# Kernel tuning notes

Hardware: AMD Instinct MI355X
Metric: run time of the kernel (lower is better)

Reference implementation:

```python
import jax, jax.numpy as jnp
import numpy as np

B, T, E, H = 4, 4096, 1024, 64

def setup_inputs() -> dict:
    key = jax.random.key(0)
    k1, k2, k3, k4 = jax.random.split(key, 4)
    x = jax.random.normal(k1, (B, T, E), dtype=jnp.float32)
    # nn.Linear(E, H, bias=False): weight [H, E]; store as [E, H] for x @ W
    scale = 1.0 / np.sqrt(E)
    Wk = jax.random.normal(k2, (E, H), dtype=jnp.float32) * scale
    Wq = jax.random.normal(k3, (E, H), dtype=jnp.float32) * scale
    Wv = jax.random.normal(k4, (E, H), dtype=jnp.float32) * scale
    return {"x": x, "Wk": Wk, "Wq": Wq, "Wv": Wv}

def reference(x, Wk, Wq, Wv):
    Bc, Tc, Ec = x.shape
    k = x @ Wk            # [B, T, H]
    q = x @ Wq            # [B, T, H]
    v = x @ Wv            # [B, T, H]
    # NOTE: original scales by 1/sqrt(embedding_size), not head_size
    scores = jnp.einsum('bqh,bkh->bqk', q, k) / jnp.sqrt(jnp.float32(Ec))
    causal = jnp.tril(jnp.ones((Tc, Tc), dtype=bool))
    scores = jnp.where(causal, scores, -jnp.inf)
    weights = jax.nn.softmax(scores, axis=-1)
    return jnp.einsum('bqk,bkh->bqh', weights, v)
```

## Files before the change

kernel.cpp:

```cpp
#include <hip/hip_runtime.h>

#define B_ 4
#define T_ 4096
#define E_ 1024
#define H_ 64

typedef __attribute__((ext_vector_type(8))) short short8;
typedef __attribute__((ext_vector_type(4))) float f32x4;

static __device__ __forceinline__ unsigned short f2bf(float f) {
    unsigned int u = __builtin_bit_cast(unsigned int, f);
    u += 0x7fffu + ((u >> 16) & 1u);
    return (unsigned short)(u >> 16);
}
static __device__ __forceinline__ float bf2f(unsigned short h) {
    unsigned int u = ((unsigned int)h) << 16;
    return __builtin_bit_cast(float, u);
}
#if __has_builtin(__builtin_amdgcn_exp2f)
#define EXP2(x) __builtin_amdgcn_exp2f(x)
#else
#define EXP2(x) exp2f(x)
#endif

#define GLOBAL_AS __attribute__((address_space(1)))
#define LDS_AS    __attribute__((address_space(3)))

__global__ __launch_bounds__(256) void wt_fragmajor_kernel(
    const float* __restrict__ Wq, const float* __restrict__ Wk,
    const float* __restrict__ Wv, unsigned short* __restrict__ Wtf)
{
    const int mat = blockIdx.x >> 4;
    const int kt  = blockIdx.x & 15;
    const float* W = (mat == 0) ? Wq : ((mat == 1) ? Wk : Wv);
    const int tid = threadIdx.x;
    const int col = tid & 63;
    const int kr  = tid >> 6;
    const int n   = col >> 4, c = col & 15;
    #pragma unroll
    for (int p = 0; p < 16; ++p) {
        const int k = kt * 64 + p * 4 + kr;
        const float v = W[k * 64 + col];
        const int q = k >> 5, g = (k >> 3) & 3, j = k & 7;
        Wtf[(((mat * 4 + n) * 32 + q) << 9) + (g * 16 + c) * 8 + j] = f2bf(v);
    }
}

__global__ __launch_bounds__(384, 4) void proj_kernel(
    const float* __restrict__ x, const unsigned short* __restrict__ Wtf,
    unsigned short* __restrict__ Qb, unsigned short* __restrict__ Kb,
    unsigned short* __restrict__ Vt)
{
    __shared__ float x_lds[2][2048];
    const int tid  = threadIdx.x;
    const int wid  = tid >> 6, lane = tid & 63;
    const int g    = lane >> 4, c = lane & 15;
    const int mat  = wid >> 1;
    const int rg   = wid & 1;
    const int r0   = blockIdx.x * 32;
    const float QSCALE = 0.03125f * 1.44269504088896f;

    auto stage = [&](int buf, int kk) {
        {
            int row = tid >> 4, ch = tid & 15;
            int csw = ch ^ (row & 15);
            const float* src = x + (size_t)(r0 + row) * E_ + kk + csw * 4;
            __builtin_amdgcn_global_load_lds(
                (const GLOBAL_AS unsigned int*)src,
                (LDS_AS unsigned int*)&x_lds[buf][(tid & ~63) * 4], 16, 0, 0);
        }
        if (tid < 128) {
            int idx2 = 384 + tid;
            int row2 = idx2 >> 4, ch2 = idx2 & 15;
            int csw2 = ch2 ^ (row2 & 15);
            const float* src2 = x + (size_t)(r0 + row2) * E_ + kk + csw2 * 4;
            __builtin_amdgcn_global_load_lds(
                (const GLOBAL_AS unsigned int*)src2,
                (LDS_AS unsigned int*)&x_lds[buf][(idx2 & ~63) * 4], 16, 0, 0);
        }
    };

    f32x4 acc[4];
    #pragma unroll
    for (int n = 0; n < 4; ++n) acc[n] = 0.0f;

    const int xrowbase = (rg * 16 + c) * 64;
    const unsigned short* wf = Wtf + (size_t)mat * 65536 + lane * 8;

    auto computeStep = [&](int buf, int t) {
        #pragma unroll
        for (int kc = 0; kc < 2; ++kc) {
            const int q = t * 2 + kc;
            f32x4 xa = *(const f32x4*)&x_lds[buf][xrowbase + ((8 * kc + 2 * g)     ^ c) * 4];
            f32x4 xb = *(const f32x4*)&x_lds[buf][xrowbase + ((8 * kc + 2 * g + 1) ^ c) * 4];
            short8 a;
            #pragma unroll
            for (int j = 0; j < 4; ++j) {
                a[j]     = (short)f2bf(xa[j]);
                a[j + 4] = (short)f2bf(xb[j]);
            }
            #pragma unroll
            for (int n = 0; n < 4; ++n) {
                short8 b = *(const short8*)&wf[n * 16384 + q * 512];
                acc[n] = __builtin_amdgcn_mfma_f32_16x16x32_bf16(a, b, acc[n], 0, 0, 0);
            }
        }
    };

    stage(0, 0);
    __syncthreads();
    for (int t = 0; t < 16; ++t) {
        const int buf = t & 1;
        if (t + 1 < 16) stage(buf ^ 1, (t + 1) * 64);
        computeStep(buf, t);
        __syncthreads();
    }

    const int bb = r0 >> 12;
    #pragma unroll
    for (int n = 0; n < 4; ++n)
        #pragma unroll
        for (int r = 0; r < 4; ++r) {
            int row = r0 + rg * 16 + 4 * g + r;
            int col = n * 16 + c;
            float v = acc[n][r];
            if (mat == 0)
                Qb[(size_t)row * H_ + col] = f2bf(v * QSCALE);
            else if (mat == 1)
                Kb[(size_t)row * H_ + col] = f2bf(v);
            else
                Vt[((size_t)bb * H_ + col) * T_ + (row & (T_ - 1))] = f2bf(v);
        }
}

__global__ __launch_bounds__(256, 3) void attn_split_kernel(
    const unsigned short* __restrict__ Qb, const unsigned short* __restrict__ Kb,
    const unsigned short* __restrict__ Vt, unsigned short* __restrict__ Po,
    float* __restrict__ Pl)
{
    __shared__ unsigned short K_lds[2][64][64];
    __shared__ unsigned short V_lds[2][64][64];
    __shared__ unsigned short p_lds[4][16][72];
    const int tid   = threadIdx.x;
    const int wid   = tid >> 6, lane = tid & 63;
    const int g     = lane >> 4, c = lane & 15;

    const int s     = blockIdx.x * 4 + wid;
    const int batch = s >> 11;
    const int rem   = s & 2047;
    const int ch    = rem >> 8;
    const int qt    = rem & 255;
    const int nkv   = (qt >> 2) + 1;
    if (ch * 8 >= nkv) return;
    const int nt    = min(8, nkv - ch * 8);
    const int qbase = qt * 16;
    const int lastt = nkv - 1 - ch * 8;

    const int Mm = nkv - 1, aa = Mm >> 3, rr8 = Mm & 7;
    const int npart = (nkv + 7) >> 3;
    const int slot  = batch * 1152 + 4 * (4 * aa * (aa + 1) + rr8 * (aa + 1))
                    + (qt & 3) * npart + ch;

    const int rsub = lane >> 3;
    const int csw  = (lane & 7) ^ rsub;
    const int cs0 = (g ^ (c & 7)) * 8;
    const int cs1 = ((g + 4) ^ (c & 7)) * 8;

    short8 aq0, aq1;
    {
        const unsigned short* qp = Qb + ((size_t)(batch * T_ + qbase + c)) * H_ + 8 * g;
        aq0 = *(const short8*)&qp[0];
        aq1 = *(const short8*)&qp[32];
    }

    short8 ones;
    #pragma unroll
    for (int j = 0; j < 8; ++j) ones[j] = (short)0x3F80;

    f32x4 o_acc[4];
    #pragma unroll
    for (int n = 0; n < 4; ++n) o_acc[n] = 0.0f;
    f32x4 l_acc = 0.0f;

    auto stage = [&](int buf, int gt) {
        const int key0 = gt * 64;
        #pragma unroll
        for (int j = 0; j < 2; ++j) {
            const int row = wid * 16 + j * 8;
            const unsigned short* gk = Kb
                + ((size_t)(batch * T_ + key0 + row + rsub)) * H_ + csw * 8;
            __builtin_amdgcn_global_load_lds(
                (const GLOBAL_AS unsigned int*)gk,
                (LDS_AS unsigned int*)&K_lds[buf][row][0], 16, 0, 0);
            const unsigned short* gv = Vt
                + ((size_t)(batch * H_ + row + rsub)) * T_ + key0 + csw * 8;
            __builtin_amdgcn_global_load_lds(
                (const GLOBAL_AS unsigned int*)gv,
                (LDS_AS unsigned int*)&V_lds[buf][row][0], 16, 0, 0);
        }
    };

    stage(0, ch * 8);
    __syncthreads();

    for (int t = 0; t < nt; ++t) {
        const int buf = t & 1;
        if (t + 1 < nt) stage(buf ^ 1, ch * 8 + t + 1);

        f32x4 sA[4];
        #pragma unroll
        for (int n = 0; n < 4; ++n) sA[n] = 0.0f;
        #pragma unroll
        for (int n = 0; n < 4; ++n) {
            short8 bk0 = *(const short8*)&K_lds[buf][n * 16 + c][cs0];
            short8 bk1 = *(const short8*)&K_lds[buf][n * 16 + c][cs1];
            sA[n] = __builtin_amdgcn_mfma_f32_16x16x32_bf16(aq0, bk0, sA[n], 0, 0, 0);
            sA[n] = __builtin_amdgcn_mfma_f32_16x16x32_bf16(aq1, bk1, sA[n], 0, 0, 0);
        }

        float pv[4][4];
        #pragma unroll
        for (int n = 0; n < 4; ++n)
            #pragma unroll
            for (int r = 0; r < 4; ++r)
                pv[n][r] = EXP2(sA[n][r]);
        if (t == lastt) {
            const int d = (ch * 8 + t) * 64 + c - qbase - 4 * g;
            #pragma unroll
            for (int n = 0; n < 4; ++n)
                #pragma unroll
                for (int r = 0; r < 4; ++r)
                    if (d + 16 * n > r) pv[n][r] = 0.0f;
        }

        #pragma unroll
        for (int n = 0; n < 4; ++n)
            #pragma unroll
            for (int r = 0; r < 4; ++r)
                p_lds[wid][4 * g + r][n * 16 + c] = f2bf(pv[n][r]);
        short8 pa0 = *(const short8*)&p_lds[wid][c][8 * g];
        short8 pa1 = *(const short8*)&p_lds[wid][c][32 + 8 * g];

        l_acc = __builtin_amdgcn_mfma_f32_16x16x32_bf16(pa0, ones, l_acc, 0, 0, 0);
        l_acc = __builtin_amdgcn_mfma_f32_16x16x32_bf16(pa1, ones, l_acc, 0, 0, 0);

        #pragma unroll
        for (int n = 0; n < 4; ++n) {
            short8 bv0 = *(const short8*)&V_lds[buf][n * 16 + c][cs0];
            short8 bv1 = *(const short8*)&V_lds[buf][n * 16 + c][cs1];
            o_acc[n] = __builtin_amdgcn_mfma_f32_16x16x32_bf16(pa0, bv0, o_acc[n], 0, 0, 0);
            o_acc[n] = __builtin_amdgcn_mfma_f32_16x16x32_bf16(pa1, bv1, o_acc[n], 0, 0, 0);
        }

        __syncthreads();
    }

    unsigned short* po = Po + (size_t)slot * 1024;
    #pragma unroll
    for (int n = 0; n < 4; ++n)
        #pragma unroll
        for (int r = 0; r < 4; ++r)
            po[(4 * g + r) * 64 + n * 16 + c] = f2bf(o_acc[n][r]);
    if (c == 0) {
        #pragma unroll
        for (int r = 0; r < 4; ++r)
            Pl[slot * 16 + 4 * g + r] = l_acc[r];
    }
}

__global__ __launch_bounds__(256) void attn_merge_kernel(
    const unsigned short* __restrict__ Po, const float* __restrict__ Pl,
    float* __restrict__ out)
{
    const int tid  = threadIdx.x;
    const int wid  = tid >> 6, lane = tid & 63;
    const int gi   = blockIdx.x * 4 + wid;
    const int batch = gi >> 8, qt = gi & 255;
    const int nkv  = (qt >> 2) + 1;
    const int npart = (nkv + 7) >> 3;
    const int Mm = nkv - 1, aa = Mm >> 3, rr8 = Mm & 7;
    const int slot0 = batch * 1152 + 4 * (4 * aa * (aa + 1) + rr8 * (aa + 1))
                    + (qt & 3) * npart;

    const int row = lane & 15, seg = lane >> 4;

    float lacc = 0.0f, o[16];
    #pragma unroll
    for (int k = 0; k < 16; ++k) o[k] = 0.0f;

    for (int i = 0; i < npart; ++i) {
        lacc += Pl[(slot0 + i) * 16 + row];
        const unsigned short* pp = Po + (size_t)(slot0 + i) * 1024 + row * 64 + seg * 16;
        short8 v0 = *(const short8*)&pp[0];
        short8 v1 = *(const short8*)&pp[8];
        #pragma unroll
        for (int k = 0; k < 8; ++k) {
            o[k]     += bf2f((unsigned short)v0[k]);
            o[8 + k] += bf2f((unsigned short)v1[k]);
        }
    }

    const float inv = 1.0f / lacc;
    float* op = out + ((size_t)(batch * T_ + qt * 16 + row)) * H_ + seg * 16;
    #pragma unroll
    for (int k = 0; k < 16; ++k) op[k] = o[k] * inv;
}

extern "C" void kernel_launch(void* const* d_in, const int* in_sizes, int n_in,
                              void* d_out, int out_size, void* d_ws, size_t ws_size,
                              hipStream_t stream)
{
    const float* x  = (const float*)d_in[0];
    const float* Wk = (const float*)d_in[1];
    const float* Wq = (const float*)d_in[2];
    const float* Wv = (const float*)d_in[3];
    float* out = (float*)d_out;

    unsigned short* Wtf = (unsigned short*)d_ws;
    unsigned short* Qb = Wtf + 3 * 64 * 1024;
    unsigned short* Kb = Qb + (size_t)B_ * T_ * H_;
    unsigned short* Vt = Kb + (size_t)B_ * T_ * H_;
    unsigned short* Po = Vt + (size_t)B_ * T_ * H_;
    float* Pl = (float*)(Po + (size_t)4608 * 1024);

    hipLaunchKernelGGL(wt_fragmajor_kernel, dim3(48), dim3(256), 0, stream, Wq, Wk, Wv, Wtf);
    hipLaunchKernelGGL(proj_kernel, dim3(512), dim3(384), 0, stream, x, Wtf, Qb, Kb, Vt);
    hipLaunchKernelGGL(attn_split_kernel, dim3(2048), dim3(256), 0, stream, Qb, Kb, Vt, Po, Pl);
    hipLaunchKernelGGL(attn_merge_kernel, dim3(256), dim3(256), 0, stream, Po, Pl, out);
}
```

Measured before the change: 68.55 us.

## Load x directly from global in projection, drop LDS staging and halve row tile

The projection kernel no longer stages x tiles into LDS with double buffering and barriers. Each wave now reads its 16 rows of x straight from global memory, converts them to bf16 and feeds the MFMAs. The block shrinks to 3 waves covering 16 rows, and the grid doubles. This removes the LDS round-trip and the synchronisation, at the cost of each of the three matrix waves re-reading the same x rows through the cache and issuing less coalesced loads.

```diff
diff --git a/kernel.cpp b/kernel.cpp
--- a/kernel.cpp
+++ b/kernel.cpp
@@ -46,74 +46,39 @@
     }
 }
 
-__global__ __launch_bounds__(384, 4) void proj_kernel(
+__global__ __launch_bounds__(192, 4) void proj_kernel(
     const float* __restrict__ x, const unsigned short* __restrict__ Wtf,
     unsigned short* __restrict__ Qb, unsigned short* __restrict__ Kb,
     unsigned short* __restrict__ Vt)
 {
-    __shared__ float x_lds[2][2048];
     const int tid  = threadIdx.x;
-    const int wid  = tid >> 6, lane = tid & 63;
+    const int mat  = tid >> 6, lane = tid & 63;
     const int g    = lane >> 4, c = lane & 15;
-    const int mat  = wid >> 1;
-    const int rg   = wid & 1;
-    const int r0   = blockIdx.x * 32;
+    const int r0   = blockIdx.x * 16;
     const float QSCALE = 0.03125f * 1.44269504088896f;
 
-    auto stage = [&](int buf, int kk) {
-        {
-            int row = tid >> 4, ch = tid & 15;
-            int csw = ch ^ (row & 15);
-            const float* src = x + (size_t)(r0 + row) * E_ + kk + csw * 4;
-            __builtin_amdgcn_global_load_lds(
-                (const GLOBAL_AS unsigned int*)src,
-                (LDS_AS unsigned int*)&x_lds[buf][(tid & ~63) * 4], 16, 0, 0);
-        }
-        if (tid < 128) {
-            int idx2 = 384 + tid;
-            int row2 = idx2 >> 4, ch2 = idx2 & 15;
-            int csw2 = ch2 ^ (row2 & 15);
-            const float* src2 = x + (size_t)(r0 + row2) * E_ + kk + csw2 * 4;
-            __builtin_amdgcn_global_load_lds(
-                (const GLOBAL_AS unsigned int*)src2,
-                (LDS_AS unsigned int*)&x_lds[buf][(idx2 & ~63) * 4], 16, 0, 0);
-        }
-    };
+    const float* xrow = x + (size_t)(r0 + c) * E_;
+    const unsigned short* wf = Wtf + (size_t)mat * 65536 + lane * 8;
 
     f32x4 acc[4];
     #pragma unroll
     for (int n = 0; n < 4; ++n) acc[n] = 0.0f;
 
-    const int xrowbase = (rg * 16 + c) * 64;
-    const unsigned short* wf = Wtf + (size_t)mat * 65536 + lane * 8;
-
-    auto computeStep = [&](int buf, int t) {
-        #pragma unroll
-        for (int kc = 0; kc < 2; ++kc) {
-            const int q = t * 2 + kc;
-            f32x4 xa = *(const f32x4*)&x_lds[buf][xrowbase + ((8 * kc + 2 * g)     ^ c) * 4];
-            f32x4 xb = *(const f32x4*)&x_lds[buf][xrowbase + ((8 * kc + 2 * g + 1) ^ c) * 4];
-            short8 a;
-            #pragma unroll
-            for (int j = 0; j < 4; ++j) {
-                a[j]     = (short)f2bf(xa[j]);
-                a[j + 4] = (short)f2bf(xb[j]);
-            }
-            #pragma unroll
-            for (int n = 0; n < 4; ++n) {
-                short8 b = *(const short8*)&wf[n * 16384 + q * 512];
-                acc[n] = __builtin_amdgcn_mfma_f32_16x16x32_bf16(a, b, acc[n], 0, 0, 0);
-            }
-        }
-    };
-
-    stage(0, 0);
-    __syncthreads();
-    for (int t = 0; t < 16; ++t) {
-        const int buf = t & 1;
-        if (t + 1 < 16) stage(buf ^ 1, (t + 1) * 64);
-        computeStep(buf, t);
-        __syncthreads();
+    #pragma unroll 8
+    for (int q = 0; q < 32; ++q) {
+        f32x4 xa = *(const f32x4*)&xrow[q * 32 + 8 * g];
+        f32x4 xb = *(const f32x4*)&xrow[q * 32 + 8 * g + 4];
+        short8 a;
+        #pragma unroll
+        for (int j = 0; j < 4; ++j) {
+            a[j]     = (short)f2bf(xa[j]);
+            a[j + 4] = (short)f2bf(xb[j]);
+        }
+        #pragma unroll
+        for (int n = 0; n < 4; ++n) {
+            short8 b = *(const short8*)&wf[n * 16384 + q * 512];
+            acc[n] = __builtin_amdgcn_mfma_f32_16x16x32_bf16(a, b, acc[n], 0, 0, 0);
+        }
     }
 
     const int bb = r0 >> 12;
@@ -121,7 +86,7 @@
     for (int n = 0; n < 4; ++n)
         #pragma unroll
         for (int r = 0; r < 4; ++r) {
-            int row = r0 + rg * 16 + 4 * g + r;
+            int row = r0 + 4 * g + r;
             int col = n * 16 + c;
             float v = acc[n][r];
             if (mat == 0)
@@ -324,7 +289,7 @@
     float* Pl = (float*)(Po + (size_t)4608 * 1024);
 
     hipLaunchKernelGGL(wt_fragmajor_kernel, dim3(48), dim3(256), 0, stream, Wq, Wk, Wv, Wtf);
-    hipLaunchKernelGGL(proj_kernel, dim3(512), dim3(384), 0, stream, x, Wtf, Qb, Kb, Vt);
+    hipLaunchKernelGGL(proj_kernel, dim3(1024), dim3(192), 0, stream, x, Wtf, Qb, Kb, Vt);
     hipLaunchKernelGGL(attn_split_kernel, dim3(2048), dim3(256), 0, stream, Qb, Kb, Vt, Po, Pl);
     hipLaunchKernelGGL(attn_merge_kernel, dim3(256), dim3(256), 0, stream, Po, Pl, out);
 }
```

After: 79.21 us. 15.6% more time.
